# Kernel optimization log

Measured on AMD Instinct MI355X. Metric: run time of the kernel, lower is better.

The kernel has to match this reference:

```python
import jax, jax.numpy as jnp
import numpy as np

B, IN_DIM, CTRL, N_LOC, LOC_SZ, OUT = 2048, 512, 512, 65536, 64, 1
EPS = 1e-8


def setup_inputs() -> dict:
    key = jax.random.key(0)
    ks = jax.random.split(key, 11)
    s = 0.02
    return {
        "x": jax.random.normal(ks[0], (B, IN_DIM), dtype=jnp.float32),
        # Controller: h = tanh(x W_h + b_h), gate = x W_g + b_g
        "W_h": jax.random.normal(ks[1], (IN_DIM, CTRL), dtype=jnp.float32) * s,
        "b_h": jnp.zeros((CTRL,), dtype=jnp.float32),
        "W_g": jax.random.normal(ks[2], (IN_DIM, 1), dtype=jnp.float32) * s,
        "b_g": jnp.zeros((1,), dtype=jnp.float32),
        # Head read-key net: key = tanh(h W_k + b_k)
        "W_k": jax.random.normal(ks[3], (CTRL, LOC_SZ), dtype=jnp.float32) * s,
        "b_k": jnp.zeros((LOC_SZ,), dtype=jnp.float32),
        # Memory matrix [locations, location_size]
        "M": jax.random.normal(ks[4], (N_LOC, LOC_SZ), dtype=jnp.float32),
        # Output linear: (ctrl_dim + location_size) -> output_dim
        "W_out": jax.random.normal(ks[5], (CTRL + LOC_SZ, OUT), dtype=jnp.float32) * s,
        "b_out": jnp.zeros((OUT,), dtype=jnp.float32),
    }


def reference(x, W_h, b_h, W_g, b_g, W_k, b_k, M, W_out, b_out):
    # Vectorized version of the original per-sample Python loop.
    h = jnp.tanh(x @ W_h + b_h)                # [B, ctrl_dim]
    gate = x @ W_g + b_g                       # [B, 1]
    read_key = jnp.tanh(h @ W_k + b_k)         # [B, loc_sz]
    # Cosine-similarity content addressing over memory rows.
    kn = read_key / (jnp.linalg.norm(read_key, axis=-1, keepdims=True) + EPS)
    Mn = M / (jnp.linalg.norm(M, axis=-1, keepdims=True) + EPS)
    sim = kn @ Mn.T                            # [B, locations]
    w_read = jax.nn.softmax(sim, axis=-1)      # [B, locations]
    r = w_read @ M                             # [B, loc_sz]
    feat = jnp.concatenate([h, r], axis=-1)    # [B, ctrl_dim + loc_sz]
    output = (feat @ W_out + b_out)[:, 0]      # [B]
    # Original returns last-iteration h, gate, w_read alongside output.
    return output, h[-1], gate[-1], w_read[-1]
```

## Files before the change

kernel.cpp:

```cpp
#include <hip/hip_runtime.h>

#define B_SZ 2048
#define IN_DIM 512
#define CTRL 512
#define N_LOC 65536
#define NSPLIT 128
#define LPS (N_LOC / NSPLIT)
#define EPSV 1e-8f
#define LOG2E 1.4426950408889634f

typedef __attribute__((ext_vector_type(8))) short bf16x8;
typedef __attribute__((ext_vector_type(4))) float f32x4;
typedef __attribute__((ext_vector_type(16))) float f32x16;
typedef __attribute__((ext_vector_type(4))) unsigned int u32x4;
typedef __attribute__((ext_vector_type(8))) unsigned short u16x8;

static __device__ __forceinline__ unsigned int cvtpk(float lo, float hi) {
  unsigned int r;
  asm("v_cvt_pk_bf16_f32 %0, %1, %2" : "=v"(r) : "v"(lo), "v"(hi));
  return r;
}
static __device__ __forceinline__ unsigned short f2bf_hw(float f) {
  return (unsigned short)(cvtpk(f, f) & 0xffffu);
}
static __device__ __forceinline__ float bf2f(unsigned short u) {
  return __builtin_bit_cast(float, ((unsigned int)u) << 16);
}
static __device__ __forceinline__ float exp2_fast(float x) {
  float r;
  asm("v_exp_f32 %0, %1" : "=v"(r) : "v"(x));
  return r;
}

__global__ __launch_bounds__(256) void k_prep_all(const float* __restrict__ x,
                                                  const float* __restrict__ Wh,
                                                  const float* __restrict__ Wk,
                                                  const float* __restrict__ M,
                                                  unsigned short* __restrict__ xb,
                                                  unsigned short* __restrict__ Wht,
                                                  unsigned short* __restrict__ Wkt,
                                                  unsigned short* __restrict__ Mn_t,
                                                  unsigned short* __restrict__ Mt_t) {
  const int bx = blockIdx.x, t = threadIdx.x;
  if (bx < 512) {
    const int base = bx * 2048 + t * 8;
    const float4 a = *(const float4*)&x[base];
    const float4 b = *(const float4*)&x[base + 4];
    u16x8 o;
    unsigned int u0 = cvtpk(a.x, a.y), u1 = cvtpk(a.z, a.w);
    unsigned int u2 = cvtpk(b.x, b.y), u3 = cvtpk(b.z, b.w);
    o[0] = (unsigned short)u0; o[1] = (unsigned short)(u0 >> 16);
    o[2] = (unsigned short)u1; o[3] = (unsigned short)(u1 >> 16);
    o[4] = (unsigned short)u2; o[5] = (unsigned short)(u2 >> 16);
    o[6] = (unsigned short)u3; o[7] = (unsigned short)(u3 >> 16);
    *(u16x8*)&xb[base] = o;
  } else if (bx < 584) {
    __shared__ float ld[64][65];
    const bool isWh = bx < 576;
    const int id = isWh ? bx - 512 : bx - 576;
    const int ti = isWh ? (id >> 3) : id;
    const int tj = isWh ? (id & 7) : 0;
    const int ncol = isWh ? CTRL : 64;
    const float* src = isWh ? Wh : Wk;
#pragma unroll
    for (int i = 0; i < 4; i++) {
      const int c = t + i * 256;
      const int r = c >> 4, c4 = (c & 15) * 4;
      const float4 v = *(const float4*)&src[(size_t)(ti * 64 + r) * ncol + tj * 64 + c4];
      ld[r][c4] = v.x; ld[r][c4 + 1] = v.y; ld[r][c4 + 2] = v.z; ld[r][c4 + 3] = v.w;
    }
    __syncthreads();
    unsigned short* dst = isWh ? Wht : Wkt;
#pragma unroll
    for (int i = 0; i < 2; i++) {
      const int c = t + i * 256;
      const int col = c >> 3, k8 = (c & 7) * 8;
      u16x8 o;
#pragma unroll
      for (int j = 0; j < 4; j++) {
        unsigned int u = cvtpk(ld[k8 + 2 * j][col], ld[k8 + 2 * j + 1][col]);
        o[2 * j] = (unsigned short)u;
        o[2 * j + 1] = (unsigned short)(u >> 16);
      }
      *(u16x8*)&dst[(size_t)(tj * 64 + col) * IN_DIM + ti * 64 + k8] = o;
    }
  } else {
    const int b = bx - 584;
    const int c4 = t & 15, lg = t >> 4;
    float vv[4][4], ss[4];
#pragma unroll
    for (int r = 0; r < 4; r++) {
      const int loc = b * 64 + lg * 4 + r;
      const float4 f = *(const float4*)&M[(size_t)loc * 64 + c4 * 4];
      vv[r][0] = f.x; vv[r][1] = f.y; vv[r][2] = f.z; vv[r][3] = f.w;
      ss[r] = f.x * f.x + f.y * f.y + f.z * f.z + f.w * f.w;
    }
#pragma unroll
    for (int r = 0; r < 4; r++)
#pragma unroll
      for (int off = 1; off < 16; off <<= 1) ss[r] += __shfl_xor(ss[r], off);
#pragma unroll
    for (int r = 0; r < 4; r++) {
      const float s = (1.f / (sqrtf(ss[r]) + EPSV)) * LOG2E;
      uint2 u;
      u.x = cvtpk(vv[r][0] * s, vv[r][1] * s);
      u.y = cvtpk(vv[r][2] * s, vv[r][3] * s);
      *(uint2*)&Mn_t[(size_t)b * 4096 + (lg * 4 + r) * 64 + c4 * 4] = u;
    }
#pragma unroll
    for (int j = 0; j < 4; j++) {
      uint2 u;
      u.x = cvtpk(vv[0][j], vv[1][j]);
      u.y = cvtpk(vv[2][j], vv[3][j]);
      *(uint2*)&Mt_t[(size_t)b * 4096 + (c4 * 4 + j) * 64 + lg * 4] = u;
    }
  }
}

__global__ __launch_bounds__(256) void k_hgemm(const unsigned short* __restrict__ xb,
                                               const unsigned short* __restrict__ Wht,
                                               const float* __restrict__ bh,
                                               float* __restrict__ h) {
  __shared__ __align__(16) unsigned short xs[64 * 32];
  __shared__ __align__(16) unsigned short wsb[64 * 32];
  const int t = threadIdx.x, lane = t & 63, w = t >> 6, lo = lane & 15, g = lane >> 4;
  const int bm = blockIdx.x * 64, bn = blockIdx.y * 64;
  f32x4 acc[4];
#pragma unroll
  for (int rt = 0; rt < 4; rt++) acc[rt] = (f32x4){0.f, 0.f, 0.f, 0.f};

  for (int k0 = 0; k0 < IN_DIM; k0 += 32) {
    {
      const int r = t >> 2, k8 = (t & 3) * 8;
      *(u16x8*)&xs[r * 32 + (k8 ^ ((r & 3) * 8))] =
          *(const u16x8*)&xb[(size_t)(bm + r) * IN_DIM + k0 + k8];
      *(u16x8*)&wsb[r * 32 + (k8 ^ ((r & 3) * 8))] =
          *(const u16x8*)&Wht[(size_t)(bn + r) * IN_DIM + k0 + k8];
    }
    __syncthreads();
    const int koff = (8 * g) ^ ((lo & 3) * 8);
    const bf16x8 bfr = *(const bf16x8*)&wsb[(16 * w + lo) * 32 + koff];
#pragma unroll
    for (int rt = 0; rt < 4; rt++) {
      const bf16x8 afr = *(const bf16x8*)&xs[(16 * rt + lo) * 32 + koff];
      acc[rt] = __builtin_amdgcn_mfma_f32_16x16x32_bf16(afr, bfr, acc[rt], 0, 0, 0);
    }
    __syncthreads();
  }
  const int col = bn + 16 * w + lo;
  const float b = bh[col];
#pragma unroll
  for (int rt = 0; rt < 4; rt++)
#pragma unroll
    for (int q = 0; q < 4; q++) {
      const int row = bm + 16 * rt + 4 * g + q;
      h[(size_t)row * CTRL + col] = tanhf(acc[rt][q] + b);
    }
}

__global__ __launch_bounds__(256) void k_readkey(const float* __restrict__ h_,
                                                 const unsigned short* __restrict__ Wkt,
                                                 const float* __restrict__ bk,
                                                 const float* __restrict__ x,
                                                 const float* __restrict__ Wg,
                                                 const float* __restrict__ bg,
                                                 unsigned short* __restrict__ kn_bf,
                                                 float* __restrict__ out) {
  __shared__ float sAcc[4][32][65];
  __shared__ float red[4];
  const int t = threadIdx.x, lane = t & 63, w = t >> 6;
  const int l31 = lane & 31, hh = lane >> 5;
  if (blockIdx.x < 64) {
    const int row0 = blockIdx.x * 32;
    f32x16 acc[2];
    acc[0] = (f32x16)(0.f); acc[1] = (f32x16)(0.f);
#pragma unroll
    for (int kk = 0; kk < 8; kk++) {
      const int kb = 128 * w + 16 * kk + 8 * hh;
      const float4 a0 = *(const float4*)&h_[(size_t)(row0 + l31) * CTRL + kb];
      const float4 a1 = *(const float4*)&h_[(size_t)(row0 + l31) * CTRL + kb + 4];
      const u32x4 av = {cvtpk(a0.x, a0.y), cvtpk(a0.z, a0.w), cvtpk(a1.x, a1.y), cvtpk(a1.z, a1.w)};
      const bf16x8 afr = __builtin_bit_cast(bf16x8, av);
#pragma unroll
      for (int ct = 0; ct < 2; ct++) {
        const bf16x8 bfr = *(const bf16x8*)&Wkt[(size_t)(32 * ct + l31) * IN_DIM + kb];
        acc[ct] = __builtin_amdgcn_mfma_f32_32x32x16_bf16(afr, bfr, acc[ct], 0, 0, 0);
      }
    }
#pragma unroll
    for (int ct = 0; ct < 2; ct++)
#pragma unroll
      for (int r = 0; r < 16; r++)
        sAcc[w][(r & 3) + 8 * (r >> 2) + 4 * hh][32 * ct + l31] = acc[ct][r];
    __syncthreads();
    const int row = t >> 3, c8 = (t & 7) * 8;
    float v[8];
    float ss = 0.f;
#pragma unroll
    for (int j = 0; j < 8; j++) {
      const float s = sAcc[0][row][c8 + j] + sAcc[1][row][c8 + j] +
                      sAcc[2][row][c8 + j] + sAcc[3][row][c8 + j] + bk[c8 + j];
      v[j] = tanhf(s);
      ss += v[j] * v[j];
    }
    ss += __shfl_xor(ss, 1);
    ss += __shfl_xor(ss, 2);
    ss += __shfl_xor(ss, 4);
    const float inv = 1.f / (sqrtf(ss) + EPSV);
    u16x8 o;
#pragma unroll
    for (int j = 0; j < 4; j++) {
      const unsigned int u = cvtpk(v[2 * j] * inv, v[2 * j + 1] * inv);
      o[2 * j] = (unsigned short)u;
      o[2 * j + 1] = (unsigned short)(u >> 16);
    }
    *(u16x8*)&kn_bf[(size_t)(row0 + row) * 64 + c8] = o;
  } else {
    out[2048 + t] = h_[(size_t)(B_SZ - 1) * CTRL + t];
    out[2048 + 256 + t] = h_[(size_t)(B_SZ - 1) * CTRL + 256 + t];
    float p = x[(size_t)(B_SZ - 1) * IN_DIM + t] * Wg[t] +
              x[(size_t)(B_SZ - 1) * IN_DIM + 256 + t] * Wg[256 + t];
#pragma unroll
    for (int off = 32; off >= 1; off >>= 1) p += __shfl_xor(p, off);
    if ((t & 63) == 0) red[t >> 6] = p;
    __syncthreads();
    if (t == 0) out[2048 + 512] = red[0] + red[1] + red[2] + red[3] + bg[0];
  }
}

__global__ __launch_bounds__(256, 2) void k_attn(const unsigned short* __restrict__ kn_bf,
                                                 const unsigned short* __restrict__ Mn_t,
                                                 const unsigned short* __restrict__ Mt_t,
                                                 float* __restrict__ l_part,
                                                 unsigned short* __restrict__ r_bf,
                                                 float* __restrict__ wdump) {
  __shared__ __align__(16) unsigned short sMn[2][4096];
  __shared__ __align__(16) unsigned short sMt[2][4096];
  const int sp = blockIdx.x, rb = blockIdx.y;
  const int t = threadIdx.x, lane = t & 63, w = t >> 6;
  const int l31 = lane & 31, hh = lane >> 5, l7 = lane & 7;
  const int row0 = rb * 256 + 64 * w;

  bf16x8 bq[2][4];
#pragma unroll
  for (int rs = 0; rs < 2; rs++)
#pragma unroll
    for (int kk = 0; kk < 4; kk++)
      bq[rs][kk] =
          *(const bf16x8*)&kn_bf[(size_t)(row0 + 32 * rs + l31) * 64 + 16 * kk + 8 * hh];

  const int c0 = t, c1 = t + 256;
  const int r0 = c0 >> 3, d0 = r0 * 64 + (((c0 & 7) * 8) ^ ((r0 & 7) * 8));
  const int r1 = c1 >> 3, d1 = r1 * 64 + (((c1 & 7) * 8) ^ ((r1 & 7) * 8));
  {
    const size_t gb = (size_t)(sp * 8) * 4096;
    *(u16x8*)&sMn[0][d0] = *(const u16x8*)&Mn_t[gb + c0 * 8];
    *(u16x8*)&sMn[0][d1] = *(const u16x8*)&Mn_t[gb + c1 * 8];
    *(u16x8*)&sMt[0][d0] = *(const u16x8*)&Mt_t[gb + c0 * 8];
    *(u16x8*)&sMt[0][d1] = *(const u16x8*)&Mt_t[gb + c1 * 8];
  }
  __syncthreads();

  f32x16 Racc[2][2];
#pragma unroll
  for (int rs = 0; rs < 2; rs++)
#pragma unroll
    for (int dt = 0; dt < 2; dt++) Racc[rs][dt] = (f32x16)(0.f);
  float lr0a = 0.f, lr0b = 0.f, lr1a = 0.f, lr1b = 0.f;

  u16x8 rn0, rn1, rt0, rt1;
  for (int it = 0; it < 8; ++it) {
    const int cur = it & 1;
    if (it < 7) {
      const size_t gn = (size_t)(sp * 8 + it + 1) * 4096;
      rn0 = *(const u16x8*)&Mn_t[gn + c0 * 8];
      rn1 = *(const u16x8*)&Mn_t[gn + c1 * 8];
      rt0 = *(const u16x8*)&Mt_t[gn + c0 * 8];
      rt1 = *(const u16x8*)&Mt_t[gn + c1 * 8];
    }

    f32x16 cst[2][2];
#pragma unroll
    for (int rs = 0; rs < 2; rs++)
#pragma unroll
      for (int lt = 0; lt < 2; lt++) cst[rs][lt] = (f32x16)(0.f);
    __builtin_amdgcn_s_setprio(1);
#pragma unroll
    for (int kk = 0; kk < 4; kk++) {
      const int koff = ((2 * kk + hh) ^ l7) * 8;
      const bf16x8 a0 = *(const bf16x8*)&sMn[cur][l31 * 64 + koff];
      const bf16x8 a1 = *(const bf16x8*)&sMn[cur][(32 + l31) * 64 + koff];
      cst[0][0] = __builtin_amdgcn_mfma_f32_32x32x16_bf16(a0, bq[0][kk], cst[0][0], 0, 0, 0);
      cst[0][1] = __builtin_amdgcn_mfma_f32_32x32x16_bf16(a1, bq[0][kk], cst[0][1], 0, 0, 0);
      cst[1][0] = __builtin_amdgcn_mfma_f32_32x32x16_bf16(a0, bq[1][kk], cst[1][0], 0, 0, 0);
      cst[1][1] = __builtin_amdgcn_mfma_f32_32x32x16_bf16(a1, bq[1][kk], cst[1][1], 0, 0, 0);
    }
    __builtin_amdgcn_s_setprio(0);

#pragma unroll
    for (int r = 0; r < 16; r++) {
      cst[0][0][r] = exp2_fast(cst[0][0][r]); lr0a += cst[0][0][r];
      cst[0][1][r] = exp2_fast(cst[0][1][r]); lr0b += cst[0][1][r];
      cst[1][0][r] = exp2_fast(cst[1][0][r]); lr1a += cst[1][0][r];
      cst[1][1][r] = exp2_fast(cst[1][1][r]); lr1b += cst[1][1][r];
    }

    if (rb == 7 && w == 3 && l31 == 31) {
#pragma unroll
      for (int lt = 0; lt < 2; lt++)
#pragma unroll
        for (int rr = 0; rr < 4; rr++)
          *(float4*)&wdump[sp * 512 + it * 64 + 32 * lt + 8 * rr + 4 * hh] =
              make_float4(cst[1][lt][4 * rr], cst[1][lt][4 * rr + 1], cst[1][lt][4 * rr + 2],
                          cst[1][lt][4 * rr + 3]);
    }

    unsigned int pkq[2][2][8];
#pragma unroll
    for (int rs = 0; rs < 2; rs++)
#pragma unroll
      for (int lt = 0; lt < 2; lt++)
#pragma unroll
        for (int m = 0; m < 8; m++)
          pkq[rs][lt][m] = cvtpk(cst[rs][lt][2 * m], cst[rs][lt][2 * m + 1]);

#pragma unroll
    for (int kk = 0; kk < 4; kk++) {
      const int lt = kk >> 1, e4 = (kk & 1) * 4;
      const int koff = ((2 * kk + hh) ^ l7) * 8;
      const bf16x8 b0f = *(const bf16x8*)&sMt[cur][l31 * 64 + koff];
      const bf16x8 b1f = *(const bf16x8*)&sMt[cur][(32 + l31) * 64 + koff];
      __builtin_amdgcn_s_setprio(1);
#pragma unroll
      for (int rs = 0; rs < 2; rs++) {
        auto s0 = __builtin_amdgcn_permlane32_swap(pkq[rs][lt][e4 + 2], pkq[rs][lt][e4 + 0],
                                                   false, false);
        auto s1 = __builtin_amdgcn_permlane32_swap(pkq[rs][lt][e4 + 3], pkq[rs][lt][e4 + 1],
                                                   false, false);
        const u32x4 aw = {(unsigned int)s0[1], (unsigned int)s1[1], (unsigned int)s0[0],
                          (unsigned int)s1[0]};
        const bf16x8 afr = __builtin_bit_cast(bf16x8, aw);
        Racc[rs][0] = __builtin_amdgcn_mfma_f32_32x32x16_bf16(afr, b0f, Racc[rs][0], 0, 0, 0);
        Racc[rs][1] = __builtin_amdgcn_mfma_f32_32x32x16_bf16(afr, b1f, Racc[rs][1], 0, 0, 0);
      }
      __builtin_amdgcn_s_setprio(0);
    }

    if (it < 7) {
      const int nxt = cur ^ 1;
      *(u16x8*)&sMn[nxt][d0] = rn0; *(u16x8*)&sMn[nxt][d1] = rn1;
      *(u16x8*)&sMt[nxt][d0] = rt0; *(u16x8*)&sMt[nxt][d1] = rt1;
    }
    __syncthreads();
  }

  float lr0 = lr0a + lr0b, lr1 = lr1a + lr1b;
  lr0 += __shfl_xor(lr0, 32);
  lr1 += __shfl_xor(lr1, 32);
  if (hh == 0) {
    l_part[(size_t)(row0 + l31) * NSPLIT + sp] = lr0;
    l_part[(size_t)(row0 + 32 + l31) * NSPLIT + sp] = lr1;
  }

#pragma unroll
  for (int rs = 0; rs < 2; rs++)
#pragma unroll
    for (int dt = 0; dt < 2; dt++)
#pragma unroll
      for (int r = 0; r < 16; r++) {
        const int brow = (r & 3) + 8 * (r >> 2) + 4 * hh;
        r_bf[((size_t)(row0 + 32 * rs + brow) * NSPLIT + sp) * 64 + 32 * dt + l31] =
            f2bf_hw(Racc[rs][dt][r]);
      }
}

__global__ __launch_bounds__(256) void k_post(const float* __restrict__ l_part,
                                              const unsigned short* __restrict__ r_bf,
                                              const float* __restrict__ h,
                                              const float* __restrict__ Wout,
                                              const float* __restrict__ bout,
                                              const float* __restrict__ wdump,
                                              float* __restrict__ out) {
  const int lane = threadIdx.x & 63, w = threadIdx.x >> 6;
  const int bx = blockIdx.x;
  if (bx < 512) {
    const int row = bx * 4 + w;
    float l = l_part[(size_t)row * NSPLIT + lane] + l_part[(size_t)row * NSPLIT + 64 + lane];
#pragma unroll
    for (int off = 32; off >= 1; off >>= 1) l += __shfl_xor(l, off);
    float rd = 0.f;
    for (int sp2 = 0; sp2 < NSPLIT; sp2++)
      rd += bf2f(r_bf[((size_t)row * NSPLIT + sp2) * 64 + lane]);
    rd /= l;
    float acc = Wout[CTRL + lane] * rd;
    for (int k = lane; k < CTRL; k += 64) acc += h[(size_t)row * CTRL + k] * Wout[k];
#pragma unroll
    for (int off = 32; off >= 1; off >>= 1) acc += __shfl_xor(acc, off);
    if (lane == 0) out[row] = acc + bout[0];
  } else {
    float l = l_part[(size_t)(B_SZ - 1) * NSPLIT + lane] +
              l_part[(size_t)(B_SZ - 1) * NSPLIT + 64 + lane];
#pragma unroll
    for (int off = 32; off >= 1; off >>= 1) l += __shfl_xor(l, off);
    const float rl = 1.f / l;
    const int i = ((bx - 512) * 256 + threadIdx.x) * 4;
    const float4 v = *(const float4*)&wdump[i];
    *(float4*)&out[2048 + 512 + 1 + i] = make_float4(v.x * rl, v.y * rl, v.z * rl, v.w * rl);
  }
}

extern "C" void kernel_launch(void* const* d_in, const int* in_sizes, int n_in,
                              void* d_out, int out_size, void* d_ws, size_t ws_size,
                              hipStream_t stream) {
  const float* x = (const float*)d_in[0];
  const float* Wh = (const float*)d_in[1];
  const float* bh = (const float*)d_in[2];
  const float* Wg = (const float*)d_in[3];
  const float* bg = (const float*)d_in[4];
  const float* Wk = (const float*)d_in[5];
  const float* bk = (const float*)d_in[6];
  const float* M = (const float*)d_in[7];
  const float* Wout = (const float*)d_in[8];
  const float* bout = (const float*)d_in[9];
  float* out = (float*)d_out;

  float* ws = (float*)d_ws;
  float* h = ws;
  float* l_part = h + 1048576;
  float* wdump = l_part + 262144;
  unsigned short* r_bf = (unsigned short*)(wdump + 65536);
  unsigned short* kn_bf = r_bf + 16777216;
  unsigned short* Mn_t = kn_bf + 131072;
  unsigned short* Mt_t = Mn_t + 4194304;
  unsigned short* xb = Mt_t + 4194304;
  unsigned short* Wht = xb + 1048576;
  unsigned short* Wkt = Wht + 262144;

  hipLaunchKernelGGL(k_prep_all, dim3(1608), dim3(256), 0, stream,
                     x, Wh, Wk, M, xb, Wht, Wkt, Mn_t, Mt_t);
  hipLaunchKernelGGL(k_hgemm, dim3(32, 8), dim3(256), 0, stream, xb, Wht, bh, h);
  hipLaunchKernelGGL(k_readkey, dim3(65), dim3(256), 0, stream,
                     h, Wkt, bk, x, Wg, bg, kn_bf, out);
  hipLaunchKernelGGL(k_attn, dim3(NSPLIT, 8), dim3(256), 0, stream,
                     kn_bf, Mn_t, Mt_t, l_part, r_bf, wdump);
  hipLaunchKernelGGL(k_post, dim3(512 + 64), dim3(256), 0, stream,
                     l_part, r_bf, h, Wout, bout, wdump, out);
}
```

Before: 83.54 us.

## Fuse prep and h-GEMM into one kernel, use direct global-to-LDS loads in attention

Merges the preprocessing kernel and the h GEMM into a single launch. The GEMM now converts fp32 x and Wh to bf16 on the fly instead of reading pre-converted copies, which removes the xb/Wht intermediates and one kernel boundary. Mn_t/Mt_t are written already in the swizzled LDS layout, so the attention kernel can double-buffer them with global_load_lds straight into shared memory, with no register staging. The bf16 packing for the R MFMA is also done inline per k-step rather than all up front, to lower register pressure. In exchange, the GEMM does redundant fp32 loads and conversions and scalar transposed LDS stores, and a full vmcnt wait is added before each barrier.

```diff
diff --git a/kernel.cpp b/kernel.cpp
--- a/kernel.cpp
+++ b/kernel.cpp
@@ -5,7 +5,6 @@
 #define CTRL 512
 #define N_LOC 65536
 #define NSPLIT 128
-#define LPS (N_LOC / NSPLIT)
 #define EPSV 1e-8f
 #define LOG2E 1.4426950408889634f
 
@@ -31,61 +30,24 @@
   asm("v_exp_f32 %0, %1" : "=v"(r) : "v"(x));
   return r;
 }
-
-__global__ __launch_bounds__(256) void k_prep_all(const float* __restrict__ x,
-                                                  const float* __restrict__ Wh,
-                                                  const float* __restrict__ Wk,
-                                                  const float* __restrict__ M,
-                                                  unsigned short* __restrict__ xb,
-                                                  unsigned short* __restrict__ Wht,
-                                                  unsigned short* __restrict__ Wkt,
-                                                  unsigned short* __restrict__ Mn_t,
-                                                  unsigned short* __restrict__ Mt_t) {
+static __device__ __forceinline__ void gld_lds16(const unsigned short* g, unsigned short* l) {
+  __builtin_amdgcn_global_load_lds(
+      (const __attribute__((address_space(1))) void*)g,
+      (__attribute__((address_space(3))) void*)l, 16, 0, 0);
+}
+
+__global__ __launch_bounds__(256) void k_mega(const float* __restrict__ x,
+                                              const float* __restrict__ Wh,
+                                              const float* __restrict__ Wk,
+                                              const float* __restrict__ M,
+                                              const float* __restrict__ bh,
+                                              unsigned short* __restrict__ Wkt,
+                                              unsigned short* __restrict__ Mn_t,
+                                              unsigned short* __restrict__ Mt_t,
+                                              float* __restrict__ h) {
   const int bx = blockIdx.x, t = threadIdx.x;
-  if (bx < 512) {
-    const int base = bx * 2048 + t * 8;
-    const float4 a = *(const float4*)&x[base];
-    const float4 b = *(const float4*)&x[base + 4];
-    u16x8 o;
-    unsigned int u0 = cvtpk(a.x, a.y), u1 = cvtpk(a.z, a.w);
-    unsigned int u2 = cvtpk(b.x, b.y), u3 = cvtpk(b.z, b.w);
-    o[0] = (unsigned short)u0; o[1] = (unsigned short)(u0 >> 16);
-    o[2] = (unsigned short)u1; o[3] = (unsigned short)(u1 >> 16);
-    o[4] = (unsigned short)u2; o[5] = (unsigned short)(u2 >> 16);
-    o[6] = (unsigned short)u3; o[7] = (unsigned short)(u3 >> 16);
-    *(u16x8*)&xb[base] = o;
-  } else if (bx < 584) {
-    __shared__ float ld[64][65];
-    const bool isWh = bx < 576;
-    const int id = isWh ? bx - 512 : bx - 576;
-    const int ti = isWh ? (id >> 3) : id;
-    const int tj = isWh ? (id & 7) : 0;
-    const int ncol = isWh ? CTRL : 64;
-    const float* src = isWh ? Wh : Wk;
-#pragma unroll
-    for (int i = 0; i < 4; i++) {
-      const int c = t + i * 256;
-      const int r = c >> 4, c4 = (c & 15) * 4;
-      const float4 v = *(const float4*)&src[(size_t)(ti * 64 + r) * ncol + tj * 64 + c4];
-      ld[r][c4] = v.x; ld[r][c4 + 1] = v.y; ld[r][c4 + 2] = v.z; ld[r][c4 + 3] = v.w;
-    }
-    __syncthreads();
-    unsigned short* dst = isWh ? Wht : Wkt;
-#pragma unroll
-    for (int i = 0; i < 2; i++) {
-      const int c = t + i * 256;
-      const int col = c >> 3, k8 = (c & 7) * 8;
-      u16x8 o;
-#pragma unroll
-      for (int j = 0; j < 4; j++) {
-        unsigned int u = cvtpk(ld[k8 + 2 * j][col], ld[k8 + 2 * j + 1][col]);
-        o[2 * j] = (unsigned short)u;
-        o[2 * j + 1] = (unsigned short)(u >> 16);
-      }
-      *(u16x8*)&dst[(size_t)(tj * 64 + col) * IN_DIM + ti * 64 + k8] = o;
-    }
-  } else {
-    const int b = bx - 584;
+  if (bx < 1024) {
+    const int b = bx;
     const int c4 = t & 15, lg = t >> 4;
     float vv[4][4], ss[4];
 #pragma unroll
@@ -101,61 +63,96 @@
       for (int off = 1; off < 16; off <<= 1) ss[r] += __shfl_xor(ss[r], off);
 #pragma unroll
     for (int r = 0; r < 4; r++) {
+      const int rr = lg * 4 + r;
       const float s = (1.f / (sqrtf(ss[r]) + EPSV)) * LOG2E;
       uint2 u;
       u.x = cvtpk(vv[r][0] * s, vv[r][1] * s);
       u.y = cvtpk(vv[r][2] * s, vv[r][3] * s);
-      *(uint2*)&Mn_t[(size_t)b * 4096 + (lg * 4 + r) * 64 + c4 * 4] = u;
+      const int pos = b * 4096 + rr * 64 + (((c4 >> 1) ^ (rr & 7)) * 8) + (c4 & 1) * 4;
+      *(uint2*)&Mn_t[pos] = u;
     }
 #pragma unroll
     for (int j = 0; j < 4; j++) {
+      const int rr = c4 * 4 + j;
       uint2 u;
       u.x = cvtpk(vv[0][j], vv[1][j]);
       u.y = cvtpk(vv[2][j], vv[3][j]);
-      *(uint2*)&Mt_t[(size_t)b * 4096 + (c4 * 4 + j) * 64 + lg * 4] = u;
-    }
-  }
-}
-
-__global__ __launch_bounds__(256) void k_hgemm(const unsigned short* __restrict__ xb,
-                                               const unsigned short* __restrict__ Wht,
-                                               const float* __restrict__ bh,
-                                               float* __restrict__ h) {
-  __shared__ __align__(16) unsigned short xs[64 * 32];
-  __shared__ __align__(16) unsigned short wsb[64 * 32];
-  const int t = threadIdx.x, lane = t & 63, w = t >> 6, lo = lane & 15, g = lane >> 4;
-  const int bm = blockIdx.x * 64, bn = blockIdx.y * 64;
-  f32x4 acc[4];
-#pragma unroll
-  for (int rt = 0; rt < 4; rt++) acc[rt] = (f32x4){0.f, 0.f, 0.f, 0.f};
-
-  for (int k0 = 0; k0 < IN_DIM; k0 += 32) {
-    {
-      const int r = t >> 2, k8 = (t & 3) * 8;
-      *(u16x8*)&xs[r * 32 + (k8 ^ ((r & 3) * 8))] =
-          *(const u16x8*)&xb[(size_t)(bm + r) * IN_DIM + k0 + k8];
-      *(u16x8*)&wsb[r * 32 + (k8 ^ ((r & 3) * 8))] =
-          *(const u16x8*)&Wht[(size_t)(bn + r) * IN_DIM + k0 + k8];
+      const int pos = b * 4096 + rr * 64 + (((lg >> 1) ^ (rr & 7)) * 8) + (lg & 1) * 4;
+      *(uint2*)&Mt_t[pos] = u;
+    }
+  } else if (bx < 1032) {
+    __shared__ float ld[64][65];
+    const int ti = bx - 1024;
+#pragma unroll
+    for (int i = 0; i < 4; i++) {
+      const int c = t + i * 256;
+      const int r = c >> 4, cc4 = (c & 15) * 4;
+      const float4 v = *(const float4*)&Wk[(size_t)(ti * 64 + r) * 64 + cc4];
+      ld[r][cc4] = v.x; ld[r][cc4 + 1] = v.y; ld[r][cc4 + 2] = v.z; ld[r][cc4 + 3] = v.w;
     }
     __syncthreads();
-    const int koff = (8 * g) ^ ((lo & 3) * 8);
-    const bf16x8 bfr = *(const bf16x8*)&wsb[(16 * w + lo) * 32 + koff];
-#pragma unroll
-    for (int rt = 0; rt < 4; rt++) {
-      const bf16x8 afr = *(const bf16x8*)&xs[(16 * rt + lo) * 32 + koff];
-      acc[rt] = __builtin_amdgcn_mfma_f32_16x16x32_bf16(afr, bfr, acc[rt], 0, 0, 0);
-    }
-    __syncthreads();
-  }
-  const int col = bn + 16 * w + lo;
-  const float b = bh[col];
-#pragma unroll
-  for (int rt = 0; rt < 4; rt++)
-#pragma unroll
-    for (int q = 0; q < 4; q++) {
-      const int row = bm + 16 * rt + 4 * g + q;
-      h[(size_t)row * CTRL + col] = tanhf(acc[rt][q] + b);
-    }
+#pragma unroll
+    for (int i = 0; i < 2; i++) {
+      const int c = t + i * 256;
+      const int col = c >> 3, k8 = (c & 7) * 8;
+      u16x8 o;
+#pragma unroll
+      for (int j = 0; j < 4; j++) {
+        unsigned int u = cvtpk(ld[k8 + 2 * j][col], ld[k8 + 2 * j + 1][col]);
+        o[2 * j] = (unsigned short)u;
+        o[2 * j + 1] = (unsigned short)(u >> 16);
+      }
+      *(u16x8*)&Wkt[(size_t)col * IN_DIM + ti * 64 + k8] = o;
+    }
+  } else {
+    __shared__ __align__(16) unsigned short xs[64 * 40];
+    __shared__ __align__(16) unsigned short whs[64 * 40];
+    const int id2 = bx - 1032;
+    const int bm = (id2 & 31) * 64, bn = (id2 >> 5) * 64;
+    const int lane = t & 63, wv = t >> 6, lo = lane & 15, g = lane >> 4;
+    f32x4 acc[4];
+#pragma unroll
+    for (int ct = 0; ct < 4; ct++) acc[ct] = (f32x4){0.f, 0.f, 0.f, 0.f};
+    for (int k0 = 0; k0 < IN_DIM; k0 += 32) {
+#pragma unroll
+      for (int i = 0; i < 2; i++) {
+        const int lin = t + i * 256;
+        const int r = lin >> 3, q = lin & 7;
+        const float4 v = *(const float4*)&x[(size_t)(bm + r) * IN_DIM + k0 + q * 4];
+        uint2 u;
+        u.x = cvtpk(v.x, v.y);
+        u.y = cvtpk(v.z, v.w);
+        *(uint2*)&xs[r * 40 + q * 4] = u;
+      }
+#pragma unroll
+      for (int i = 0; i < 2; i++) {
+        const int lin = t + i * 256;
+        const int kk = lin >> 4, q = lin & 15;
+        const float4 v = *(const float4*)&Wh[(size_t)(k0 + kk) * CTRL + bn + q * 4];
+        const unsigned int a = cvtpk(v.x, v.y), b2 = cvtpk(v.z, v.w);
+        whs[(q * 4 + 0) * 40 + kk] = (unsigned short)a;
+        whs[(q * 4 + 1) * 40 + kk] = (unsigned short)(a >> 16);
+        whs[(q * 4 + 2) * 40 + kk] = (unsigned short)b2;
+        whs[(q * 4 + 3) * 40 + kk] = (unsigned short)(b2 >> 16);
+      }
+      __syncthreads();
+      const bf16x8 afr = *(const bf16x8*)&xs[(16 * wv + lo) * 40 + 8 * g];
+#pragma unroll
+      for (int ct = 0; ct < 4; ct++) {
+        const bf16x8 bfr = *(const bf16x8*)&whs[(16 * ct + lo) * 40 + 8 * g];
+        acc[ct] = __builtin_amdgcn_mfma_f32_16x16x32_bf16(afr, bfr, acc[ct], 0, 0, 0);
+      }
+      __syncthreads();
+    }
+#pragma unroll
+    for (int ct = 0; ct < 4; ct++)
+#pragma unroll
+      for (int q = 0; q < 4; q++) {
+        const int row = bm + 16 * wv + 4 * g + q;
+        const int col = bn + 16 * ct + lo;
+        h[(size_t)row * CTRL + col] = tanhf(acc[ct][q] + bh[col]);
+      }
+  }
 }
 
 __global__ __launch_bounds__(256) void k_readkey(const float* __restrict__ h_,
@@ -249,16 +246,17 @@
       bq[rs][kk] =
           *(const bf16x8*)&kn_bf[(size_t)(row0 + 32 * rs + l31) * 64 + 16 * kk + 8 * hh];
 
-  const int c0 = t, c1 = t + 256;
-  const int r0 = c0 >> 3, d0 = r0 * 64 + (((c0 & 7) * 8) ^ ((r0 & 7) * 8));
-  const int r1 = c1 >> 3, d1 = r1 * 64 + (((c1 & 7) * 8) ^ ((r1 & 7) * 8));
+  const int so = w * 1024 + lane * 8;
+  const int lo0 = w * 1024;
   {
     const size_t gb = (size_t)(sp * 8) * 4096;
-    *(u16x8*)&sMn[0][d0] = *(const u16x8*)&Mn_t[gb + c0 * 8];
-    *(u16x8*)&sMn[0][d1] = *(const u16x8*)&Mn_t[gb + c1 * 8];
-    *(u16x8*)&sMt[0][d0] = *(const u16x8*)&Mt_t[gb + c0 * 8];
-    *(u16x8*)&sMt[0][d1] = *(const u16x8*)&Mt_t[gb + c1 * 8];
-  }
+#pragma unroll
+    for (int cc = 0; cc < 2; cc++) {
+      gld_lds16(&Mn_t[gb + so + cc * 512], &sMn[0][lo0 + cc * 512]);
+      gld_lds16(&Mt_t[gb + so + cc * 512], &sMt[0][lo0 + cc * 512]);
+    }
+  }
+  asm volatile("s_waitcnt vmcnt(0)" ::: "memory");
   __syncthreads();
 
   f32x16 Racc[2][2];
@@ -268,15 +266,15 @@
     for (int dt = 0; dt < 2; dt++) Racc[rs][dt] = (f32x16)(0.f);
   float lr0a = 0.f, lr0b = 0.f, lr1a = 0.f, lr1b = 0.f;
 
-  u16x8 rn0, rn1, rt0, rt1;
   for (int it = 0; it < 8; ++it) {
-    const int cur = it & 1;
+    const int cur = it & 1, nxt = cur ^ 1;
     if (it < 7) {
       const size_t gn = (size_t)(sp * 8 + it + 1) * 4096;
-      rn0 = *(const u16x8*)&Mn_t[gn + c0 * 8];
-      rn1 = *(const u16x8*)&Mn_t[gn + c1 * 8];
-      rt0 = *(const u16x8*)&Mt_t[gn + c0 * 8];
-      rt1 = *(const u16x8*)&Mt_t[gn + c1 * 8];
+#pragma unroll
+      for (int cc = 0; cc < 2; cc++) {
+        gld_lds16(&Mn_t[gn + so + cc * 512], &sMn[nxt][lo0 + cc * 512]);
+        gld_lds16(&Mt_t[gn + so + cc * 512], &sMt[nxt][lo0 + cc * 512]);
+      }
     }
 
     f32x16 cst[2][2];
@@ -315,42 +313,31 @@
                           cst[1][lt][4 * rr + 3]);
     }
 
-    unsigned int pkq[2][2][8];
-#pragma unroll
-    for (int rs = 0; rs < 2; rs++)
-#pragma unroll
-      for (int lt = 0; lt < 2; lt++)
-#pragma unroll
-        for (int m = 0; m < 8; m++)
-          pkq[rs][lt][m] = cvtpk(cst[rs][lt][2 * m], cst[rs][lt][2 * m + 1]);
-
+    __builtin_amdgcn_s_setprio(1);
 #pragma unroll
     for (int kk = 0; kk < 4; kk++) {
-      const int lt = kk >> 1, e4 = (kk & 1) * 4;
+      const int lt = kk >> 1, e8 = (kk & 1) * 8;
       const int koff = ((2 * kk + hh) ^ l7) * 8;
       const bf16x8 b0f = *(const bf16x8*)&sMt[cur][l31 * 64 + koff];
       const bf16x8 b1f = *(const bf16x8*)&sMt[cur][(32 + l31) * 64 + koff];
-      __builtin_amdgcn_s_setprio(1);
 #pragma unroll
       for (int rs = 0; rs < 2; rs++) {
-        auto s0 = __builtin_amdgcn_permlane32_swap(pkq[rs][lt][e4 + 2], pkq[rs][lt][e4 + 0],
-                                                   false, false);
-        auto s1 = __builtin_amdgcn_permlane32_swap(pkq[rs][lt][e4 + 3], pkq[rs][lt][e4 + 1],
-                                                   false, false);
+        const unsigned int p0 = cvtpk(cst[rs][lt][e8 + 0], cst[rs][lt][e8 + 1]);
+        const unsigned int p1 = cvtpk(cst[rs][lt][e8 + 2], cst[rs][lt][e8 + 3]);
+        const unsigned int p2 = cvtpk(cst[rs][lt][e8 + 4], cst[rs][lt][e8 + 5]);
+        const unsigned int p3 = cvtpk(cst[rs][lt][e8 + 6], cst[rs][lt][e8 + 7]);
+        auto s0 = __builtin_amdgcn_permlane32_swap(p2, p0, false, false);
+        auto s1 = __builtin_amdgcn_permlane32_swap(p3, p1, false, false);
         const u32x4 aw = {(unsigned int)s0[1], (unsigned int)s1[1], (unsigned int)s0[0],
                           (unsigned int)s1[0]};
         const bf16x8 afr = __builtin_bit_cast(bf16x8, aw);
         Racc[rs][0] = __builtin_amdgcn_mfma_f32_32x32x16_bf16(afr, b0f, Racc[rs][0], 0, 0, 0);
         Racc[rs][1] = __builtin_amdgcn_mfma_f32_32x32x16_bf16(afr, b1f, Racc[rs][1], 0, 0, 0);
       }
-      __builtin_amdgcn_s_setprio(0);
-    }
-
-    if (it < 7) {
-      const int nxt = cur ^ 1;
-      *(u16x8*)&sMn[nxt][d0] = rn0; *(u16x8*)&sMn[nxt][d1] = rn1;
-      *(u16x8*)&sMt[nxt][d0] = rt0; *(u16x8*)&sMt[nxt][d1] = rt1;
-    }
+    }
+    __builtin_amdgcn_s_setprio(0);
+
+    asm volatile("s_waitcnt vmcnt(0)" ::: "memory");
     __syncthreads();
   }
 
@@ -432,13 +419,10 @@
   unsigned short* kn_bf = r_bf + 16777216;
   unsigned short* Mn_t = kn_bf + 131072;
   unsigned short* Mt_t = Mn_t + 4194304;
-  unsigned short* xb = Mt_t + 4194304;
-  unsigned short* Wht = xb + 1048576;
-  unsigned short* Wkt = Wht + 262144;
-
-  hipLaunchKernelGGL(k_prep_all, dim3(1608), dim3(256), 0, stream,
-                     x, Wh, Wk, M, xb, Wht, Wkt, Mn_t, Mt_t);
-  hipLaunchKernelGGL(k_hgemm, dim3(32, 8), dim3(256), 0, stream, xb, Wht, bh, h);
+  unsigned short* Wkt = Mt_t + 4194304;
+
+  hipLaunchKernelGGL(k_mega, dim3(1288), dim3(256), 0, stream,
+                     x, Wh, Wk, M, bh, Wkt, Mn_t, Mt_t, h);
   hipLaunchKernelGGL(k_readkey, dim3(65), dim3(256), 0, stream,
                      h, Wkt, bk, x, Wg, bg, kn_bf, out);
   hipLaunchKernelGGL(k_attn, dim3(NSPLIT, 8), dim3(256), 0, stream,
```

Result: slower. 85.32 us (+2.1%).
